# Performance work log

Measured on AMD Instinct MI355X. Metric: run time of the kernel, lower is better.

Reference implementation:

```python
import jax, jax.numpy as jnp
import numpy as np

B, T, I, S, H = 32, 8192, 256, 256, 256
NEG = 1e30


def setup_inputs() -> dict:
    key = jax.random.key(0)
    ks = jax.random.split(key, 8)
    x = jax.random.normal(ks[0], (B, T, I), dtype=jnp.float32)
    init = jax.random.normal(ks[1], (B, S), dtype=jnp.float32)
    mask = (jax.random.uniform(ks[2], (B, T)) > 0.1).astype(jnp.float32)
    W1 = jax.random.normal(ks[3], (H, S + I), dtype=jnp.float32) * (1.0 / np.sqrt(S + I))
    W2 = jax.random.normal(ks[4], (1, H), dtype=jnp.float32) * (1.0 / np.sqrt(H))
    w_ih = jax.random.normal(ks[5], (3 * S, I), dtype=jnp.float32) * (1.0 / np.sqrt(I))
    w_hh = jax.random.normal(ks[6], (3 * S, S), dtype=jnp.float32) * (1.0 / np.sqrt(S))
    b_ih = jnp.zeros((3 * S,), dtype=jnp.float32)
    b_hh = jnp.zeros((3 * S,), dtype=jnp.float32)
    return {"x": x, "init": init, "mask": mask, "W1": W1, "W2": W2,
            "w_ih": w_ih, "w_hh": w_hh, "b_ih": b_ih, "b_hh": b_hh}


def _pointer(x, state, mask, W1, W2):
    # concat([state_expanded, input], dim=2) @ W1.T == state @ W1[:, :S].T + x @ W1[:, S:].T
    Ws, Wi = W1[:, :S], W1[:, S:]
    h = jnp.tanh(jnp.einsum('bti,hi->bth', x, Wi) + (state @ Ws.T)[:, None, :])  # [B,T,H]
    att = jnp.einsum('bth,oh->bto', h, W2)[..., 0]  # [B,T]
    logit = att - NEG * (1.0 - mask)
    p = jax.nn.softmax(logit, axis=1)
    out = jnp.einsum('bt,bti->bi', p, x)
    return out, logit


def _gru_cell(inp, h, w_ih, w_hh, b_ih, b_hh):
    gi = inp @ w_ih.T + b_ih  # [B, 3S]
    gh = h @ w_hh.T + b_hh
    i_r, i_z, i_n = jnp.split(gi, 3, axis=1)
    h_r, h_z, h_n = jnp.split(gh, 3, axis=1)
    r = jax.nn.sigmoid(i_r + h_r)
    z = jax.nn.sigmoid(i_z + h_z)
    n = jnp.tanh(i_n + r * h_n)
    return (1.0 - z) * n + z * h


def reference(x, init, mask, W1, W2, w_ih, w_hh, b_ih, b_hh):
    # eval mode: all dropout masks are identity (dropout=0.0)
    out, logit1 = _pointer(x, init, mask, W1, W2)
    state = _gru_cell(out, init, w_ih, w_hh, b_ih, b_hh)
    _, logit2 = _pointer(x, state, mask, W1, W2)
    return (logit1, logit2)
```

## Files before the change

kernel.cpp:

```cpp
#include <hip/hip_runtime.h>
#include <hip/hip_bf16.h>
#include <stdint.h>

#define BB 32
#define TT 8192
#define II 256
#define SS 256
#define HH 256
#define NEGC 1e30f

typedef __bf16 bf16x8 __attribute__((ext_vector_type(8)));
typedef __bf16 bf16x4 __attribute__((ext_vector_type(4)));
typedef float f32x4 __attribute__((ext_vector_type(4)));

__device__ __forceinline__ float fast_tanh(float x) {
    float e = __expf(2.f * x);
    return 1.f - 2.f / (e + 1.f);
}

__global__ __launch_bounds__(256) void wi_cvt_kernel(const float* __restrict__ W1,
                                                     __bf16* __restrict__ wi) {
    int idx = blockIdx.x * 256 + threadIdx.x;
    int h = idx >> 8, k = idx & 255;
    wi[idx] = (__bf16)W1[h * 512 + 256 + k];
}

__global__ __launch_bounds__(256) void sws_kernel(const float* __restrict__ state,
                                                  const float* __restrict__ W1,
                                                  float* __restrict__ sws) {
    int b = blockIdx.x, tid = threadIdx.x;
    __shared__ float sv[256];
    sv[tid] = state[b * 256 + tid];
    __syncthreads();
    const float* w1r = W1 + (size_t)tid * 512;
    float a = 0.f;
#pragma unroll 8
    for (int s = 0; s < 256; ++s) a += sv[s] * w1r[s];
    sws[b * 256 + tid] = a;
}

template <int MODE>
__global__ __launch_bounds__(256, 2) void att_kernel(
    const float* __restrict__ x, const __bf16* __restrict__ xbf_in,
    __bf16* __restrict__ xbf_out, const __bf16* __restrict__ wi,
    const float* __restrict__ w2, const float* __restrict__ sws,
    const float* __restrict__ mask, float* __restrict__ logit_out) {
    __shared__ char xs[64 * 512];
    __shared__ float attp[4][64];

    const int tid = threadIdx.x;
    const int lane = tid & 63, w = tid >> 6;
    const size_t rowbase = (size_t)blockIdx.x * 64;
    const int b = (int)(rowbase >> 13);

    if (MODE == 1) {
        const char* src = (const char*)xbf_in + rowbase * 512;
#pragma unroll
        for (int it = 0; it < 8; ++it) {
            int L = (it * 256 + tid) * 16;
            bf16x8 v = *(const bf16x8*)(src + L);
            int row = L >> 9, kb = L & 511;
            *(bf16x8*)(xs + row * 512 + (kb ^ ((row & 7) << 4))) = v;
        }
    } else {
        const float* src = x + rowbase * 256;
#pragma unroll
        for (int it = 0; it < 8; ++it) {
            int L = (it * 256 + tid) * 16;
            int e = L >> 1;
            float4 f0 = *(const float4*)(src + e);
            float4 f1 = *(const float4*)(src + e + 4);
            bf16x8 v;
            v[0] = (__bf16)f0.x; v[1] = (__bf16)f0.y; v[2] = (__bf16)f0.z; v[3] = (__bf16)f0.w;
            v[4] = (__bf16)f1.x; v[5] = (__bf16)f1.y; v[6] = (__bf16)f1.z; v[7] = (__bf16)f1.w;
            int row = L >> 9, kb = L & 511;
            *(bf16x8*)(xs + row * 512 + (kb ^ ((row & 7) << 4))) = v;
            if (MODE == 0)
                *(bf16x8*)((char*)xbf_out + rowbase * 512 + L) = v;
        }
    }
    __syncthreads();

    const int l15 = lane & 15, lg = lane >> 4;
    f32x4 acc[4][4] = {};
    const char* wib = (const char*)wi + (size_t)(w * 64 + l15) * 512 + lg * 16;
#pragma unroll
    for (int kk = 0; kk < 8; ++kk) {
        bf16x8 bfrag[4];
#pragma unroll
        for (int fn = 0; fn < 4; ++fn)
            bfrag[fn] = *(const bf16x8*)(wib + fn * 16 * 512 + kk * 64);
        bf16x8 afrag[4];
#pragma unroll
        for (int fm = 0; fm < 4; ++fm) {
            int row = fm * 16 + l15;
            int kb = kk * 64 + lg * 16;
            afrag[fm] = *(const bf16x8*)(xs + row * 512 + (kb ^ ((row & 7) << 4)));
        }
#pragma unroll
        for (int fm = 0; fm < 4; ++fm)
#pragma unroll
            for (int fn = 0; fn < 4; ++fn)
                acc[fm][fn] = __builtin_amdgcn_mfma_f32_16x16x32_bf16(
                    afrag[fm], bfrag[fn], acc[fm][fn], 0, 0, 0);
    }

    float w2v[4], swsv[4];
#pragma unroll
    for (int fn = 0; fn < 4; ++fn) {
        int h = w * 64 + fn * 16 + l15;
        w2v[fn] = w2[h];
        swsv[fn] = sws[b * 256 + h];
    }
#pragma unroll
    for (int fm = 0; fm < 4; ++fm) {
        float part[4];
#pragma unroll
        for (int r = 0; r < 4; ++r) {
            float s = 0.f;
#pragma unroll
            for (int fn = 0; fn < 4; ++fn) {
                float hv = acc[fm][fn][r] + swsv[fn];
                s += w2v[fn] * fast_tanh(hv);
            }
            part[r] = s;
        }
#pragma unroll
        for (int m = 1; m < 16; m <<= 1)
#pragma unroll
            for (int r = 0; r < 4; ++r) part[r] += __shfl_xor(part[r], m, 64);
        if (l15 == 0) {
#pragma unroll
            for (int r = 0; r < 4; ++r) attp[w][fm * 16 + lg * 4 + r] = part[r];
        }
    }
    __syncthreads();
    if (tid < 64) {
        float att = attp[0][tid] + attp[1][tid] + attp[2][tid] + attp[3][tid];
        float mv = mask[rowbase + tid];
        logit_out[rowbase + tid] = att - NEGC * (1.f - mv);
    }
}

__global__ __launch_bounds__(256) void softmax_kernel(const float* __restrict__ logit,
                                                      float* __restrict__ p) {
    __shared__ float lbuf[TT];
    __shared__ float red[4], red2[4];
    int b = blockIdx.x, tid = threadIdx.x;
    const float* lp = logit + (size_t)b * TT;
    float m = -3.4e38f;
    for (int t = tid; t < TT; t += 256) {
        float v = lp[t];
        lbuf[t] = v;
        m = fmaxf(m, v);
    }
#pragma unroll
    for (int o = 1; o < 64; o <<= 1) m = fmaxf(m, __shfl_xor(m, o, 64));
    if ((tid & 63) == 0) red[tid >> 6] = m;
    __syncthreads();
    m = fmaxf(fmaxf(red[0], red[1]), fmaxf(red[2], red[3]));
    float s = 0.f;
    for (int t = tid; t < TT; t += 256) s += __expf(lbuf[t] - m);
#pragma unroll
    for (int o = 1; o < 64; o <<= 1) s += __shfl_xor(s, o, 64);
    if ((tid & 63) == 0) red2[tid >> 6] = s;
    __syncthreads();
    s = red2[0] + red2[1] + red2[2] + red2[3];
    float inv = 1.f / s;
    float* pp = p + (size_t)b * TT;
    for (int t = tid; t < TT; t += 256) pp[t] = __expf(lbuf[t] - m) * inv;
}

template <int MODE>
__global__ __launch_bounds__(256) void outpart_kernel(const float* __restrict__ p,
                                                      const float* __restrict__ xf,
                                                      const __bf16* __restrict__ xbf,
                                                      float* __restrict__ out_part) {
    int b = blockIdx.x >> 3, c = blockIdx.x & 7;
    int tid = threadIdx.x;
    int ig = tid & 63, tg = tid >> 6;
    __shared__ float pl[1024];
    __shared__ float sacc[4][256];
    const size_t tbase = (size_t)b * TT + (size_t)c * 1024;
    for (int t = tid; t < 1024; t += 256) pl[t] = p[tbase + t];
    __syncthreads();
    float a0 = 0, a1 = 0, a2 = 0, a3 = 0;
    if (MODE == 0) {
        const __bf16* xp = xbf + tbase * 256 + ig * 4;
        for (int t = tg; t < 1024; t += 4) {
            float pv = pl[t];
            bf16x4 v = *(const bf16x4*)(xp + (size_t)t * 256);
            a0 += pv * (float)v[0];
            a1 += pv * (float)v[1];
            a2 += pv * (float)v[2];
            a3 += pv * (float)v[3];
        }
    } else {
        const float* xp = xf + tbase * 256 + ig * 4;
        for (int t = tg; t < 1024; t += 4) {
            float pv = pl[t];
            float4 v = *(const float4*)(xp + (size_t)t * 256);
            a0 += pv * v.x;
            a1 += pv * v.y;
            a2 += pv * v.z;
            a3 += pv * v.w;
        }
    }
    sacc[tg][ig * 4 + 0] = a0;
    sacc[tg][ig * 4 + 1] = a1;
    sacc[tg][ig * 4 + 2] = a2;
    sacc[tg][ig * 4 + 3] = a3;
    __syncthreads();
    if (tid < 256) {
        float s = sacc[0][tid] + sacc[1][tid] + sacc[2][tid] + sacc[3][tid];
        out_part[(size_t)(b * 8 + c) * 256 + tid] = s;
    }
}

__global__ __launch_bounds__(256) void gru_sws_kernel(
    const float* __restrict__ out_part, const float* __restrict__ init,
    const float* __restrict__ w_ih, const float* __restrict__ w_hh,
    const float* __restrict__ b_ih, const float* __restrict__ b_hh,
    const float* __restrict__ W1, float* __restrict__ sws2) {
    int b = blockIdx.x, tid = threadIdx.x;
    __shared__ float outv[256], initv[256], statev[256];
    __shared__ float gi[768], gh[768];
    float o = 0.f;
#pragma unroll
    for (int c = 0; c < 8; ++c) o += out_part[(size_t)(b * 8 + c) * 256 + tid];
    outv[tid] = o;
    initv[tid] = init[b * 256 + tid];
    __syncthreads();
#pragma unroll
    for (int kb = 0; kb < 3; ++kb) {
        int k = kb * 256 + tid;
        const float* wir = w_ih + (size_t)k * 256;
        const float* whr = w_hh + (size_t)k * 256;
        float gia = b_ih[k], gha = b_hh[k];
#pragma unroll 8
        for (int i = 0; i < 256; ++i) {
            gia += outv[i] * wir[i];
            gha += initv[i] * whr[i];
        }
        gi[k] = gia;
        gh[k] = gha;
    }
    __syncthreads();
    {
        float r = 1.f / (1.f + __expf(-(gi[tid] + gh[tid])));
        float z = 1.f / (1.f + __expf(-(gi[256 + tid] + gh[256 + tid])));
        float n = fast_tanh(gi[512 + tid] + r * gh[512 + tid]);
        statev[tid] = (1.f - z) * n + z * initv[tid];
    }
    __syncthreads();
    {
        const float* w1r = W1 + (size_t)tid * 512;
        float a = 0.f;
#pragma unroll 8
        for (int s = 0; s < 256; ++s) a += statev[s] * w1r[s];
        sws2[b * 256 + tid] = a;
    }
}

extern "C" void kernel_launch(void* const* d_in, const int* in_sizes, int n_in,
                              void* d_out, int out_size, void* d_ws, size_t ws_size,
                              hipStream_t stream) {
    const float* x = (const float*)d_in[0];
    const float* init = (const float*)d_in[1];
    const float* mask = (const float*)d_in[2];
    const float* W1 = (const float*)d_in[3];
    const float* W2 = (const float*)d_in[4];
    const float* w_ih = (const float*)d_in[5];
    const float* w_hh = (const float*)d_in[6];
    const float* b_ih = (const float*)d_in[7];
    const float* b_hh = (const float*)d_in[8];
    float* out = (float*)d_out;

    char* ws = (char*)d_ws;
    size_t off = 0;
    auto alloc = [&](size_t sz) {
        char* p = ws + off;
        off += (sz + 255) & ~(size_t)255;
        return p;
    };
    float* p_buf = (float*)alloc((size_t)BB * TT * 4);
    __bf16* wi = (__bf16*)alloc((size_t)HH * II * 2);
    float* sws1 = (float*)alloc(BB * 256 * 4);
    float* sws2 = (float*)alloc(BB * 256 * 4);
    float* out_part = (float*)alloc(BB * 8 * 256 * 4);
    size_t small_off = off;
    __bf16* xbf = (__bf16*)alloc((size_t)BB * TT * II * 2);
    const bool big = (off <= ws_size);
    (void)small_off;
    (void)in_sizes; (void)n_in; (void)out_size;

    wi_cvt_kernel<<<256, 256, 0, stream>>>(W1, wi);
    sws_kernel<<<32, 256, 0, stream>>>(init, W1, sws1);

    const int ntiles = BB * TT / 64;
    if (big)
        att_kernel<0><<<ntiles, 256, 0, stream>>>(x, nullptr, xbf, wi, W2, sws1, mask, out);
    else
        att_kernel<2><<<ntiles, 256, 0, stream>>>(x, nullptr, nullptr, wi, W2, sws1, mask, out);

    softmax_kernel<<<32, 256, 0, stream>>>(out, p_buf);

    if (big)
        outpart_kernel<0><<<256, 256, 0, stream>>>(p_buf, nullptr, xbf, out_part);
    else
        outpart_kernel<2><<<256, 256, 0, stream>>>(p_buf, x, nullptr, out_part);

    gru_sws_kernel<<<32, 256, 0, stream>>>(out_part, init, w_ih, w_hh, b_ih, b_hh, W1, sws2);

    if (big)
        att_kernel<1><<<ntiles, 256, 0, stream>>>(nullptr, xbf, nullptr, wi, W2, sws2, mask,
                                                  out + (size_t)BB * TT);
    else
        att_kernel<2><<<ntiles, 256, 0, stream>>>(x, nullptr, nullptr, wi, W2, sws2, mask,
                                                  out + (size_t)BB * TT);
}
```

Before: 696.4 us.

## Split softmax into chunk stats, restructure GRU/sws GEMVs, trim att reductions

Replaces the per-batch softmax kernel with a 256-block chunk-statistics pass, and folds the normalization into outpart so the p buffer is no longer written or read. The GRU and state-projection GEMVs are restructured to slice over output rows across blocks, with all batches kept in padded shared memory, and the GRU is split into GEMM and pointwise kernels. The attention kernel raises its occupancy hint to 3 and replaces the butterfly shuffle reduction with a transpose-style reduction that needs fewer shuffles. Fast reciprocal intrinsics replace divisions. The small serial kernels get more parallelism, but there are more launches and the higher occupancy target may cause register spills.

```diff
diff --git a/kernel.cpp b/kernel.cpp
--- a/kernel.cpp
+++ b/kernel.cpp
@@ -15,7 +15,10 @@
 
 __device__ __forceinline__ float fast_tanh(float x) {
     float e = __expf(2.f * x);
-    return 1.f - 2.f / (e + 1.f);
+    return 1.f - 2.f * __builtin_amdgcn_rcpf(e + 1.f);
+}
+__device__ __forceinline__ float fast_sigmoid(float x) {
+    return __builtin_amdgcn_rcpf(1.f + __expf(-x));
 }
 
 __global__ __launch_bounds__(256) void wi_cvt_kernel(const float* __restrict__ W1,
@@ -25,22 +28,32 @@
     wi[idx] = (__bf16)W1[h * 512 + 256 + k];
 }
 
-__global__ __launch_bounds__(256) void sws_kernel(const float* __restrict__ state,
-                                                  const float* __restrict__ W1,
-                                                  float* __restrict__ sws) {
-    int b = blockIdx.x, tid = threadIdx.x;
-    __shared__ float sv[256];
-    sv[tid] = state[b * 256 + tid];
-    __syncthreads();
-    const float* w1r = W1 + (size_t)tid * 512;
-    float a = 0.f;
-#pragma unroll 8
-    for (int s = 0; s < 256; ++s) a += sv[s] * w1r[s];
-    sws[b * 256 + tid] = a;
+__global__ __launch_bounds__(256) void sws_slice_kernel(const float* __restrict__ state,
+                                                        const float* __restrict__ W1,
+                                                        float* __restrict__ sws) {
+    __shared__ float sv[32 * 257];
+    int tid = threadIdx.x;
+    for (int e = tid; e < 8192; e += 256) {
+        int b = e >> 8, s = e & 255;
+        sv[b * 257 + s] = state[b * 256 + s];
+    }
+    __syncthreads();
+    int hl = tid >> 4, bg = tid & 15;
+    int h = blockIdx.x * 16 + hl;
+    const float* w1r = W1 + (size_t)h * 512;
+    float a0 = 0.f, a1 = 0.f;
+#pragma unroll 4
+    for (int s = 0; s < 256; ++s) {
+        float w = w1r[s];
+        a0 += w * sv[(bg * 2 + 0) * 257 + s];
+        a1 += w * sv[(bg * 2 + 1) * 257 + s];
+    }
+    sws[(bg * 2 + 0) * 256 + h] = a0;
+    sws[(bg * 2 + 1) * 256 + h] = a1;
 }
 
 template <int MODE>
-__global__ __launch_bounds__(256, 2) void att_kernel(
+__global__ __launch_bounds__(256, 3) void att_kernel(
     const float* __restrict__ x, const __bf16* __restrict__ xbf_in,
     __bf16* __restrict__ xbf_out, const __bf16* __restrict__ wi,
     const float* __restrict__ w2, const float* __restrict__ sws,
@@ -112,6 +125,8 @@
         w2v[fn] = w2[h];
         swsv[fn] = sws[b * 256 + h];
     }
+    const bool hi8 = (l15 & 8) != 0, hi4 = (l15 & 4) != 0;
+    const int ridx = ((l15 & 8) >> 2) | ((l15 & 4) >> 2);
 #pragma unroll
     for (int fm = 0; fm < 4; ++fm) {
         float part[4];
@@ -125,14 +140,18 @@
             }
             part[r] = s;
         }
-#pragma unroll
-        for (int m = 1; m < 16; m <<= 1)
-#pragma unroll
-            for (int r = 0; r < 4; ++r) part[r] += __shfl_xor(part[r], m, 64);
-        if (l15 == 0) {
-#pragma unroll
-            for (int r = 0; r < 4; ++r) attp[w][fm * 16 + lg * 4 + r] = part[r];
-        }
+        float s0 = hi8 ? part[0] : part[2];
+        float s1 = hi8 ? part[1] : part[3];
+        float r0 = __shfl_xor(s0, 8, 64);
+        float r1 = __shfl_xor(s1, 8, 64);
+        float a0 = (hi8 ? part[2] : part[0]) + r0;
+        float a1 = (hi8 ? part[3] : part[1]) + r1;
+        float s2 = hi4 ? a0 : a1;
+        float r2 = __shfl_xor(s2, 4, 64);
+        float bsum = (hi4 ? a1 : a0) + r2;
+        bsum += __shfl_xor(bsum, 2, 64);
+        bsum += __shfl_xor(bsum, 1, 64);
+        if ((l15 & 3) == 0) attp[w][fm * 16 + lg * 4 + ridx] = bsum;
     }
     __syncthreads();
     if (tid < 64) {
@@ -142,47 +161,54 @@
     }
 }
 
-__global__ __launch_bounds__(256) void softmax_kernel(const float* __restrict__ logit,
-                                                      float* __restrict__ p) {
-    __shared__ float lbuf[TT];
-    __shared__ float red[4], red2[4];
-    int b = blockIdx.x, tid = threadIdx.x;
-    const float* lp = logit + (size_t)b * TT;
-    float m = -3.4e38f;
-    for (int t = tid; t < TT; t += 256) {
-        float v = lp[t];
-        lbuf[t] = v;
-        m = fmaxf(m, v);
-    }
+__global__ __launch_bounds__(256) void chunkstat_kernel(const float* __restrict__ logit,
+                                                        float2* __restrict__ stat) {
+    __shared__ float redm[4], reds[4];
+    int bc = blockIdx.x, tid = threadIdx.x;
+    const float* lp = logit + (size_t)bc * 1024;
+    float4 v = *(const float4*)(lp + tid * 4);
+    float m = fmaxf(fmaxf(v.x, v.y), fmaxf(v.z, v.w));
 #pragma unroll
     for (int o = 1; o < 64; o <<= 1) m = fmaxf(m, __shfl_xor(m, o, 64));
-    if ((tid & 63) == 0) red[tid >> 6] = m;
-    __syncthreads();
-    m = fmaxf(fmaxf(red[0], red[1]), fmaxf(red[2], red[3]));
-    float s = 0.f;
-    for (int t = tid; t < TT; t += 256) s += __expf(lbuf[t] - m);
+    if ((tid & 63) == 0) redm[tid >> 6] = m;
+    __syncthreads();
+    m = fmaxf(fmaxf(redm[0], redm[1]), fmaxf(redm[2], redm[3]));
+    float s = __expf(v.x - m) + __expf(v.y - m) + __expf(v.z - m) + __expf(v.w - m);
 #pragma unroll
     for (int o = 1; o < 64; o <<= 1) s += __shfl_xor(s, o, 64);
-    if ((tid & 63) == 0) red2[tid >> 6] = s;
-    __syncthreads();
-    s = red2[0] + red2[1] + red2[2] + red2[3];
-    float inv = 1.f / s;
-    float* pp = p + (size_t)b * TT;
-    for (int t = tid; t < TT; t += 256) pp[t] = __expf(lbuf[t] - m) * inv;
+    if ((tid & 63) == 0) reds[tid >> 6] = s;
+    __syncthreads();
+    if (tid == 0) {
+        float2 st;
+        st.x = m;
+        st.y = reds[0] + reds[1] + reds[2] + reds[3];
+        stat[bc] = st;
+    }
 }
 
 template <int MODE>
-__global__ __launch_bounds__(256) void outpart_kernel(const float* __restrict__ p,
-                                                      const float* __restrict__ xf,
-                                                      const __bf16* __restrict__ xbf,
-                                                      float* __restrict__ out_part) {
+__global__ __launch_bounds__(256) void outpart_kernel(
+    const float* __restrict__ logit, const float2* __restrict__ stat,
+    const float* __restrict__ xf, const __bf16* __restrict__ xbf,
+    float* __restrict__ out_part) {
     int b = blockIdx.x >> 3, c = blockIdx.x & 7;
     int tid = threadIdx.x;
     int ig = tid & 63, tg = tid >> 6;
     __shared__ float pl[1024];
     __shared__ float sacc[4][256];
+    float m = -3.4e38f;
+#pragma unroll
+    for (int cc = 0; cc < 8; ++cc) m = fmaxf(m, stat[b * 8 + cc].x);
+    float ssum = 0.f;
+#pragma unroll
+    for (int cc = 0; cc < 8; ++cc) {
+        float2 st = stat[b * 8 + cc];
+        ssum += st.y * __expf(st.x - m);
+    }
+    float invs = 1.f / ssum;
     const size_t tbase = (size_t)b * TT + (size_t)c * 1024;
-    for (int t = tid; t < 1024; t += 256) pl[t] = p[tbase + t];
+    for (int t = tid; t < 1024; t += 256)
+        pl[t] = __expf(logit[tbase + t] - m) * invs;
     __syncthreads();
     float a0 = 0, a1 = 0, a2 = 0, a3 = 0;
     if (MODE == 0) {
@@ -217,49 +243,54 @@
     }
 }
 
-__global__ __launch_bounds__(256) void gru_sws_kernel(
+__global__ __launch_bounds__(256) void gru_gemm_kernel(
     const float* __restrict__ out_part, const float* __restrict__ init,
     const float* __restrict__ w_ih, const float* __restrict__ w_hh,
     const float* __restrict__ b_ih, const float* __restrict__ b_hh,
-    const float* __restrict__ W1, float* __restrict__ sws2) {
-    int b = blockIdx.x, tid = threadIdx.x;
-    __shared__ float outv[256], initv[256], statev[256];
-    __shared__ float gi[768], gh[768];
-    float o = 0.f;
-#pragma unroll
-    for (int c = 0; c < 8; ++c) o += out_part[(size_t)(b * 8 + c) * 256 + tid];
-    outv[tid] = o;
-    initv[tid] = init[b * 256 + tid];
-    __syncthreads();
-#pragma unroll
-    for (int kb = 0; kb < 3; ++kb) {
-        int k = kb * 256 + tid;
-        const float* wir = w_ih + (size_t)k * 256;
-        const float* whr = w_hh + (size_t)k * 256;
-        float gia = b_ih[k], gha = b_hh[k];
-#pragma unroll 8
-        for (int i = 0; i < 256; ++i) {
-            gia += outv[i] * wir[i];
-            gha += initv[i] * whr[i];
-        }
-        gi[k] = gia;
-        gh[k] = gha;
-    }
-    __syncthreads();
-    {
-        float r = 1.f / (1.f + __expf(-(gi[tid] + gh[tid])));
-        float z = 1.f / (1.f + __expf(-(gi[256 + tid] + gh[256 + tid])));
-        float n = fast_tanh(gi[512 + tid] + r * gh[512 + tid]);
-        statev[tid] = (1.f - z) * n + z * initv[tid];
-    }
-    __syncthreads();
-    {
-        const float* w1r = W1 + (size_t)tid * 512;
-        float a = 0.f;
-#pragma unroll 8
-        for (int s = 0; s < 256; ++s) a += statev[s] * w1r[s];
-        sws2[b * 256 + tid] = a;
-    }
+    float* __restrict__ gi, float* __restrict__ gh) {
+    __shared__ float outv[32 * 257];
+    __shared__ float initv[32 * 257];
+    int tid = threadIdx.x;
+    for (int e = tid; e < 8192; e += 256) {
+        int b = e >> 8, i = e & 255;
+        float o = 0.f;
+#pragma unroll
+        for (int c = 0; c < 8; ++c) o += out_part[(size_t)(b * 8 + c) * 256 + i];
+        outv[b * 257 + i] = o;
+        initv[b * 257 + i] = init[b * 256 + i];
+    }
+    __syncthreads();
+    int kl = tid >> 4, bg = tid & 15;
+    int k = blockIdx.x * 16 + kl;
+    const float* wir = w_ih + (size_t)k * 256;
+    const float* whr = w_hh + (size_t)k * 256;
+    float gia0 = b_ih[k], gia1 = gia0;
+    float gha0 = b_hh[k], gha1 = gha0;
+#pragma unroll 4
+    for (int i = 0; i < 256; ++i) {
+        float wiv = wir[i], whv = whr[i];
+        gia0 += wiv * outv[(bg * 2 + 0) * 257 + i];
+        gia1 += wiv * outv[(bg * 2 + 1) * 257 + i];
+        gha0 += whv * initv[(bg * 2 + 0) * 257 + i];
+        gha1 += whv * initv[(bg * 2 + 1) * 257 + i];
+    }
+    gi[k * 32 + bg * 2 + 0] = gia0;
+    gi[k * 32 + bg * 2 + 1] = gia1;
+    gh[k * 32 + bg * 2 + 0] = gha0;
+    gh[k * 32 + bg * 2 + 1] = gha1;
+}
+
+__global__ __launch_bounds__(256) void gru_point_kernel(
+    const float* __restrict__ gi, const float* __restrict__ gh,
+    const float* __restrict__ init, float* __restrict__ state) {
+    int b = blockIdx.x, s = threadIdx.x;
+    float gir = gi[s * 32 + b], giz = gi[(256 + s) * 32 + b], gin = gi[(512 + s) * 32 + b];
+    float ghr = gh[s * 32 + b], ghz = gh[(256 + s) * 32 + b], ghn = gh[(512 + s) * 32 + b];
+    float r = fast_sigmoid(gir + ghr);
+    float z = fast_sigmoid(giz + ghz);
+    float n = fast_tanh(gin + r * ghn);
+    float h0 = init[b * 256 + s];
+    state[b * 256 + s] = (1.f - z) * n + z * h0;
 }
 
 extern "C" void kernel_launch(void* const* d_in, const int* in_sizes, int n_in,
@@ -283,19 +314,20 @@
         off += (sz + 255) & ~(size_t)255;
         return p;
     };
-    float* p_buf = (float*)alloc((size_t)BB * TT * 4);
     __bf16* wi = (__bf16*)alloc((size_t)HH * II * 2);
     float* sws1 = (float*)alloc(BB * 256 * 4);
     float* sws2 = (float*)alloc(BB * 256 * 4);
     float* out_part = (float*)alloc(BB * 8 * 256 * 4);
-    size_t small_off = off;
+    float2* stat = (float2*)alloc(BB * 8 * 8);
+    float* gi_buf = (float*)alloc(768 * 32 * 4);
+    float* gh_buf = (float*)alloc(768 * 32 * 4);
+    float* state_buf = (float*)alloc(BB * 256 * 4);
     __bf16* xbf = (__bf16*)alloc((size_t)BB * TT * II * 2);
     const bool big = (off <= ws_size);
-    (void)small_off;
     (void)in_sizes; (void)n_in; (void)out_size;
 
     wi_cvt_kernel<<<256, 256, 0, stream>>>(W1, wi);
-    sws_kernel<<<32, 256, 0, stream>>>(init, W1, sws1);
+    sws_slice_kernel<<<16, 256, 0, stream>>>(init, W1, sws1);
 
     const int ntiles = BB * TT / 64;
     if (big)
@@ -303,14 +335,17 @@
     else
         att_kernel<2><<<ntiles, 256, 0, stream>>>(x, nullptr, nullptr, wi, W2, sws1, mask, out);
 
-    softmax_kernel<<<32, 256, 0, stream>>>(out, p_buf);
+    chunkstat_kernel<<<256, 256, 0, stream>>>(out, stat);
 
     if (big)
-        outpart_kernel<0><<<256, 256, 0, stream>>>(p_buf, nullptr, xbf, out_part);
+        outpart_kernel<0><<<256, 256, 0, stream>>>(out, stat, nullptr, xbf, out_part);
     else
-        outpart_kernel<2><<<256, 256, 0, stream>>>(p_buf, x, nullptr, out_part);
-
-    gru_sws_kernel<<<32, 256, 0, stream>>>(out_part, init, w_ih, w_hh, b_ih, b_hh, W1, sws2);
+        outpart_kernel<2><<<256, 256, 0, stream>>>(out, stat, x, nullptr, out_part);
+
+    gru_gemm_kernel<<<48, 256, 0, stream>>>(out_part, init, w_ih, w_hh, b_ih, b_hh,
+                                            gi_buf, gh_buf);
+    gru_point_kernel<<<32, 256, 0, stream>>>(gi_buf, gh_buf, init, state_buf);
+    sws_slice_kernel<<<16, 256, 0, stream>>>(state_buf, W1, sws2);
 
     if (big)
         att_kernel<1><<<ntiles, 256, 0, stream>>>(nullptr, xbf, nullptr, wi, W2, sws2, mask,
```

Result: faster. 649.1 us (-6.8%).
